# Kernel tuning notes

Measured on AMD Instinct MI355X. Metric: run time of the kernel, lower is better.

## Reference

```python
import jax, jax.numpy as jnp
import numpy as np

B, N, D, H, K, T = 32, 4096, 256, 4, 8, 3
D_H = D // H
SCALE = D_H ** -0.5
EPS = 1e-8
LN_EPS = 1e-5


def _ln(x, g, b):
    m = x.mean(-1, keepdims=True)
    v = ((x - m) ** 2).mean(-1, keepdims=True)
    return (x - m) / jnp.sqrt(v + LN_EPS) * g + b


def _split(t):  # [b, n, D] -> [b, H, n, d_h]
    b, n, _ = t.shape
    return t.reshape(b, n, H, D_H).transpose(0, 2, 1, 3)


def _merge(t):  # [b, H, n, d_h] -> [b, n, D]
    b, h, n, d = t.shape
    return t.transpose(0, 2, 1, 3).reshape(b, n, h * d)


def setup_inputs() -> dict:
    key = jax.random.key(0)
    ks = jax.random.split(key, 12)
    init = lambda k, shape: (jax.random.normal(k, shape, jnp.float32) * 0.02)
    mu = jnp.tile(jnp.linspace(-1.0, 1.0, K)[:, None], (1, D))[None]  # [1,K,D]
    return {
        'x': jax.random.normal(ks[0], (B, N, D), jnp.float32),
        'mu': mu,
        'w_q': init(ks[1], (D, D)),
        'w_k': init(ks[2], (D, D)),
        'w_v': init(ks[3], (D, D)),
        'w_comb': init(ks[4], (D, D)),
        'g_in': jnp.ones(D), 'b_in': jnp.zeros(D),
        'g_slot': jnp.ones(D), 'b_slot': jnp.zeros(D),
        'g_mlp': jnp.ones(D), 'b_mlp': jnp.zeros(D),
        'w_ih': init(ks[5], (3 * D, D)),
        'w_hh': init(ks[6], (3 * D, D)),
        'b_ih': jnp.zeros(3 * D),
        'b_hh': jnp.zeros(3 * D),
        'w1': init(ks[7], (D, D)), 'b1': jnp.zeros(D),
        'w2': init(ks[8], (D, D)), 'b2': jnp.zeros(D),
    }


def reference(x, mu, w_q, w_k, w_v, w_comb, g_in, b_in, g_slot, b_slot,
              g_mlp, b_mlp, w_ih, w_hh, b_ih, b_hh, w1, b1, w2, b2):
    b = x.shape[0]
    x_norm = _ln(x, g_in, b_in)
    k_feat = _split(x_norm @ w_k.T)  # [b,H,N,d_h]
    v_feat = _split(x_norm @ w_v.T)

    def gru(u, h):  # torch GRUCell semantics
        gi = u @ w_ih.T + b_ih
        gh = h @ w_hh.T + b_hh
        ir, iz, i_n = jnp.split(gi, 3, axis=-1)
        hr, hz, h_n = jnp.split(gh, 3, axis=-1)
        r = jax.nn.sigmoid(ir + hr)
        z = jax.nn.sigmoid(iz + hz)
        n = jnp.tanh(i_n + r * h_n)
        return (1.0 - z) * n + z * h

    def step(slots, _):
        q = _split(_ln(slots, g_slot, b_slot) @ w_q.T)  # [b,H,K,d_h]
        dots = jnp.einsum('bhkd,bhnd->bhkn', q, k_feat) * SCALE
        attn = jax.nn.softmax(dots, axis=-2)  # softmax over slots
        attn = attn / (attn.sum(axis=-1, keepdims=True) + EPS)  # renorm over inputs
        updates = _merge(jnp.einsum('bhkn,bhnd->bhkd', attn, v_feat)) @ w_comb.T
        new = gru(updates.reshape(-1, D), slots.reshape(-1, D)).reshape(slots.shape)
        hid = jnp.maximum(_ln(new, g_mlp, b_mlp) @ w1.T + b1, 0.0)
        new = new + (hid @ w2.T + b2)
        return new, None

    slots0 = jnp.broadcast_to(mu, (b, K, D))  # eval mode: slots = mu
    slots, _ = jax.lax.scan(step, slots0, None, length=T)
    return slots
```

## Files before the change

kernel.cpp:

```cpp
#include <hip/hip_runtime.h>

#define BB 32
#define NN 4096
#define DD 256
#define HH 4
#define KK 8
#define DH 64

typedef unsigned short u16;
typedef unsigned int u32;
typedef __attribute__((ext_vector_type(8))) short short8;
typedef __attribute__((ext_vector_type(4))) float f32x4;

__device__ __forceinline__ float b2f(u16 u){ return __uint_as_float(((u32)u)<<16); }
__device__ __forceinline__ u16 f2b(float f){
  u32 u = __float_as_uint(f);
  u32 r = (u + 0x7fffu + ((u>>16)&1u)) >> 16;
  return (u16)r;
}

__global__ __launch_bounds__(256) void prep_kernel(
    const float* __restrict__ mu, const float* __restrict__ w_q,
    const float* __restrict__ w_k, const float* __restrict__ w_v,
    const float* __restrict__ w_comb, const float* __restrict__ w_ih,
    const float* __restrict__ w_hh, const float* __restrict__ w1,
    const float* __restrict__ w2,
    u16* __restrict__ wkv, u16* __restrict__ wq_b, u16* __restrict__ wcomb_b,
    u16* __restrict__ wih_b, u16* __restrict__ whh_b, u16* __restrict__ w1_b,
    u16* __restrict__ w2_b, float* __restrict__ slots)
{
  int i = blockIdx.x*256 + threadIdx.x;
  if (i < 131072) {
    int c = i>>8, d = i&255;
    float v = (c<256) ? w_k[c*256+d] : w_v[(c-256)*256+d];
    int off = (c<<9) + ((2*d) ^ ((c&15)<<4));
    wkv[off>>1] = f2b(v);
    return;
  }
  i -= 131072;
  if (i < 65536){ wq_b[i] = f2b(w_q[i]); return; } i -= 65536;
  if (i < 65536){ wcomb_b[i] = f2b(w_comb[i]); return; } i -= 65536;
  if (i < 196608){ wih_b[i] = f2b(w_ih[i]); return; } i -= 196608;
  if (i < 196608){ whh_b[i] = f2b(w_hh[i]); return; } i -= 196608;
  if (i < 65536){ w1_b[i] = f2b(w1[i]); return; } i -= 65536;
  if (i < 65536){ w2_b[i] = f2b(w2[i]); return; } i -= 65536;
  if (i < 65536){ slots[i] = mu[i & 2047]; return; }
}

__global__ __launch_bounds__(512) void kv_proj_kernel(
    const float* __restrict__ x, const float* __restrict__ g_in,
    const float* __restrict__ b_in, const u16* __restrict__ wkv,
    u16* __restrict__ Kmat, u16* __restrict__ Vmat)
{
  __shared__ __align__(16) u16 Atile[64*256];
  __shared__ __align__(16) u16 Btile[64*256];
  __shared__ __align__(16) u16 Cbuf[64*64];
  const int tid = threadIdx.x;
  const int w = tid>>6, l = tid&63;
  const long row0 = (long)blockIdx.x * 64;

  short8 breg[4];
  #pragma unroll
  for (int i=0;i<4;++i)
    breg[i] = *(const short8*)((const char*)wkv + (i*512 + tid)*16);

  const f32x4 gv = *(const f32x4*)(g_in + l*4);
  const f32x4 bv = *(const f32x4*)(b_in + l*4);

  #pragma unroll
  for (int rr=0; rr<8; ++rr) {
    const int r = w*8 + rr;
    const f32x4 xv = *(const f32x4*)(x + (row0+r)*DD + l*4);
    float s = xv.x+xv.y+xv.z+xv.w;
    float s2 = xv.x*xv.x+xv.y*xv.y+xv.z*xv.z+xv.w*xv.w;
    #pragma unroll
    for (int m=1;m<64;m<<=1){ s += __shfl_xor(s,m); s2 += __shfl_xor(s2,m); }
    const float mean = s * (1.f/256.f);
    const float rstd = rsqrtf(s2*(1.f/256.f) - mean*mean + 1e-5f);
    const u32 p0 = (u32)f2b((xv.x-mean)*rstd*gv.x + bv.x) | ((u32)f2b((xv.y-mean)*rstd*gv.y + bv.y)<<16);
    const u32 p1 = (u32)f2b((xv.z-mean)*rstd*gv.z + bv.z) | ((u32)f2b((xv.w-mean)*rstd*gv.w + bv.w)<<16);
    const unsigned long long pp = (unsigned long long)p0 | ((unsigned long long)p1<<32);
    *(unsigned long long*)((char*)Atile + r*512 + ((l*8) ^ ((r&15)<<4))) = pp;
  }
  #pragma unroll
  for (int i=0;i<4;++i)
    *(short8*)((char*)Btile + (i*512+tid)*16) = breg[i];
  __syncthreads();

  const int wm = w>>2, wn = w&3;
  const int lr = l&15;
  const int lk = (l>>4)*8;

  for (int ct=0; ct<8; ++ct) {
    short8 nreg[4];
    if (ct < 7) {
      #pragma unroll
      for (int i=0;i<4;++i)
        nreg[i] = *(const short8*)((const char*)wkv + (ct+1)*32768 + (i*512 + tid)*16);
    }

    f32x4 acc0 = (f32x4)0.f, acc1 = (f32x4)0.f;
    #pragma unroll
    for (int ks=0; ks<8; ++ks) {
      const int k2 = (ks*32 + lk)*2;
      short8 af0, af1, bfv;
      { const int r = wm*32 + lr;       af0 = *(const short8*)((const char*)Atile + r*512 + (k2 ^ ((r&15)<<4))); }
      { const int r = wm*32 + 16 + lr;  af1 = *(const short8*)((const char*)Atile + r*512 + (k2 ^ ((r&15)<<4))); }
      { const int c = wn*16 + lr;       bfv = *(const short8*)((const char*)Btile + c*512 + (k2 ^ ((c&15)<<4))); }
      acc0 = __builtin_amdgcn_mfma_f32_16x16x32_bf16(af0, bfv, acc0, 0,0,0);
      acc1 = __builtin_amdgcn_mfma_f32_16x16x32_bf16(af1, bfv, acc1, 0,0,0);
    }

    {
      const int c = wn*16 + lr;
      #pragma unroll
      for (int reg=0; reg<4; ++reg) {
        const int r0r = wm*32 + (l>>4)*4 + reg;
        const int r1r = r0r + 16;
        *(u16*)((char*)Cbuf + r0r*128 + ((2*c) ^ ((r0r&7)<<4))) = f2b(acc0[reg]);
        *(u16*)((char*)Cbuf + r1r*128 + ((2*c) ^ ((r1r&7)<<4))) = f2b(acc1[reg]);
      }
    }
    __syncthreads();

    if (ct < 7) {
      #pragma unroll
      for (int i=0;i<4;++i)
        *(short8*)((char*)Btile + (i*512+tid)*16) = nreg[i];
    }
    {
      const int r = tid>>3, cg = tid&7;
      const short8 vv = *(const short8*)((char*)Cbuf + r*128 + ((cg*16) ^ ((r&7)<<4)));
      u16* dst = (ct<4) ? Kmat : Vmat;
      *(short8*)(dst + (row0+r)*DD + (ct&3)*64 + cg*8) = vv;
    }
    __syncthreads();
  }
}

__global__ __launch_bounds__(256) void slot_q_kernel(
    const float* __restrict__ slots, const float* __restrict__ g_slot,
    const float* __restrict__ b_slot, const u16* __restrict__ wq_b,
    float* __restrict__ qmat)
{
  __shared__ float xn[256];
  __shared__ float red[8];
  const int r = blockIdx.x, t = threadIdx.x;
  const int w = t>>6, l = t&63;
  const float xv = slots[r*256 + t];
  float s = xv, s2 = xv*xv;
  #pragma unroll
  for (int m=1;m<64;m<<=1){ s += __shfl_xor(s,m); s2 += __shfl_xor(s2,m); }
  if (l==0){ red[w*2]=s; red[w*2+1]=s2; }
  __syncthreads();
  s = red[0]+red[2]+red[4]+red[6];
  s2 = red[1]+red[3]+red[5]+red[7];
  const float mean = s*(1.f/256.f);
  const float rstd = rsqrtf(s2*(1.f/256.f)-mean*mean + 1e-5f);
  xn[t] = (xv-mean)*rstd*g_slot[t] + b_slot[t];
  __syncthreads();
  const u16* wr = wq_b + t*256;
  float a0=0,a1=0,a2=0,a3=0;
  for (int d=0; d<256; d+=8) {
    const short8 wv = *(const short8*)(wr + d);
    a0 = fmaf(b2f((u16)wv[0]), xn[d+0], a0);
    a1 = fmaf(b2f((u16)wv[1]), xn[d+1], a1);
    a2 = fmaf(b2f((u16)wv[2]), xn[d+2], a2);
    a3 = fmaf(b2f((u16)wv[3]), xn[d+3], a3);
    a0 = fmaf(b2f((u16)wv[4]), xn[d+4], a0);
    a1 = fmaf(b2f((u16)wv[5]), xn[d+5], a1);
    a2 = fmaf(b2f((u16)wv[6]), xn[d+6], a2);
    a3 = fmaf(b2f((u16)wv[7]), xn[d+7], a3);
  }
  qmat[r*256 + t] = ((a0+a1)+(a2+a3));
}

__global__ __launch_bounds__(256) void attn_kernel(
    const u16* __restrict__ Kmat, const u16* __restrict__ Vmat,
    const float* __restrict__ qmat, float* __restrict__ U_part,
    float* __restrict__ S_part)
{
  __shared__ float U_lds[4][8][64];
  __shared__ float S_lds[4][8];
  const int bid = blockIdx.x;
  const int part = bid & 3, h = (bid>>2)&3, b = bid>>4;
  const int t = threadIdx.x, w = t>>6, l = t&63;
  const int ds = l&7, ng = l>>3;

  float qreg[8][8];
  #pragma unroll
  for (int k=0;k<8;++k) {
    const f32x4 qa = *(const f32x4*)(qmat + (b*8+k)*256 + h*64 + ds*8);
    const f32x4 qb = *(const f32x4*)(qmat + (b*8+k)*256 + h*64 + ds*8 + 4);
    qreg[k][0]=qa.x; qreg[k][1]=qa.y; qreg[k][2]=qa.z; qreg[k][3]=qa.w;
    qreg[k][4]=qb.x; qreg[k][5]=qb.y; qreg[k][6]=qb.z; qreg[k][7]=qb.w;
  }

  float accU[8][8];
  float sacc[8];
  #pragma unroll
  for (int k=0;k<8;++k){ sacc[k]=0.f;
    #pragma unroll
    for (int j=0;j<8;++j) accU[k][j]=0.f; }

  const long base = ((long)b*NN)*DD + h*64;
  for (int pass=0; pass<32; ++pass) {
    const int n = part*1024 + pass*32 + w*8 + ng;
    const short8 kvv = *(const short8*)(Kmat + base + (long)n*DD + ds*8);
    float kd[8];
    #pragma unroll
    for (int j=0;j<8;++j) kd[j] = b2f((u16)kvv[j]);
    float dots[8];
    #pragma unroll
    for (int k=0;k<8;++k) {
      float d0 = qreg[k][0]*kd[0] + qreg[k][1]*kd[1] + qreg[k][2]*kd[2] + qreg[k][3]*kd[3]
               + qreg[k][4]*kd[4] + qreg[k][5]*kd[5] + qreg[k][6]*kd[6] + qreg[k][7]*kd[7];
      d0 += __shfl_xor(d0,1); d0 += __shfl_xor(d0,2); d0 += __shfl_xor(d0,4);
      dots[k] = d0 * 0.125f;
    }
    float mx = dots[0];
    #pragma unroll
    for (int k=1;k<8;++k) mx = fmaxf(mx, dots[k]);
    float e[8]; float se = 0.f;
    #pragma unroll
    for (int k=0;k<8;++k){ e[k] = __expf(dots[k]-mx); se += e[k]; }
    const float inv = 1.f/se;
    const short8 vvv = *(const short8*)(Vmat + base + (long)n*DD + ds*8);
    float vd[8];
    #pragma unroll
    for (int j=0;j<8;++j) vd[j] = b2f((u16)vvv[j]);
    #pragma unroll
    for (int k=0;k<8;++k) {
      const float p = e[k]*inv;
      sacc[k] += p;
      #pragma unroll
      for (int j=0;j<8;++j) accU[k][j] = fmaf(p, vd[j], accU[k][j]);
    }
  }
  #pragma unroll
  for (int k=0;k<8;++k){
    #pragma unroll
    for (int j=0;j<8;++j){
      float v = accU[k][j];
      v += __shfl_xor(v,8); v += __shfl_xor(v,16); v += __shfl_xor(v,32);
      accU[k][j]=v;
    }
    float sv = sacc[k];
    sv += __shfl_xor(sv,8); sv += __shfl_xor(sv,16); sv += __shfl_xor(sv,32);
    sacc[k]=sv;
  }
  if (l<8){
    #pragma unroll
    for (int k=0;k<8;++k)
      #pragma unroll
      for (int j=0;j<8;++j) U_lds[w][k][l*8+j] = accU[k][j];
  }
  if (l==0){
    #pragma unroll
    for (int k=0;k<8;++k) S_lds[w][k]=sacc[k];
  }
  __syncthreads();
  for (int i=t;i<512;i+=256){
    const int k=i>>6, d=i&63;
    U_part[(((long)part*32 + b)*4 + h)*512 + k*64 + d] =
      U_lds[0][k][d]+U_lds[1][k][d]+U_lds[2][k][d]+U_lds[3][k][d];
  }
  if (t<8){
    S_part[((part*32 + b)*4 + h)*8 + t] = S_lds[0][t]+S_lds[1][t]+S_lds[2][t]+S_lds[3][t];
  }
}

__global__ __launch_bounds__(256) void slot_update_kernel(
    const float* __restrict__ U_part, const float* __restrict__ S_part,
    float* __restrict__ slots,
    const u16* __restrict__ wcomb_b, const u16* __restrict__ wih_b,
    const u16* __restrict__ whh_b, const u16* __restrict__ w1_b,
    const u16* __restrict__ w2_b,
    const float* __restrict__ b_ih, const float* __restrict__ b_hh,
    const float* __restrict__ g_mlp, const float* __restrict__ b_mlp,
    const float* __restrict__ b1v, const float* __restrict__ b2v,
    float* __restrict__ out_final, const int write_out)
{
  __shared__ float uL[2][256];
  __shared__ float hL[2][256];
  __shared__ float cL[2][256];
  __shared__ float xL[2][256];
  __shared__ float red[16];
  const int blk = blockIdx.x, t = threadIdx.x;
  const int w = t>>6, l = t&63;
  const int r0 = blk*2;

  #pragma unroll
  for (int rr=0;rr<2;++rr) hL[rr][t] = slots[(r0+rr)*256 + t];

  #pragma unroll
  for (int rr=0;rr<2;++rr) {
    const int r = r0+rr, b = r>>3, k = r&7;
    const int h = t>>6, d = t&63;
    float ssum = 0.f, usum = 0.f;
    #pragma unroll
    for (int p=0;p<4;++p) {
      ssum += S_part[((p*32 + b)*4 + h)*8 + k];
      usum += U_part[(((long)p*32 + b)*4 + h)*512 + k*64 + d];
    }
    uL[rr][t] = usum / (ssum + 1e-8f);
  }
  __syncthreads();

  {
    float c00=0,c01=0,c10=0,c11=0;
    const u16* wr = wcomb_b + t*256;
    for (int d0=0; d0<256; d0+=8) {
      const short8 wv = *(const short8*)(wr + d0);
      float wf[8];
      #pragma unroll
      for (int j=0;j<8;++j) wf[j]=b2f((u16)wv[j]);
      #pragma unroll
      for (int j=0;j<8;j+=2) {
        c00 = fmaf(wf[j],   uL[0][d0+j],   c00);
        c01 = fmaf(wf[j+1], uL[0][d0+j+1], c01);
        c10 = fmaf(wf[j],   uL[1][d0+j],   c10);
        c11 = fmaf(wf[j+1], uL[1][d0+j+1], c11);
      }
    }
    cL[0][t]=c00+c01; cL[1][t]=c10+c11;
  }
  __syncthreads();

  float gi[3][2], gh[3][2];
  #pragma unroll
  for (int g=0; g<3; ++g){ gi[g][0]=0; gi[g][1]=0; gh[g][0]=0; gh[g][1]=0; }
  for (int d0=0; d0<256; d0+=8) {
    float u0[8],u1[8],h0[8],h1[8];
    #pragma unroll
    for (int j=0;j<8;j+=4) {
      *(f32x4*)&u0[j] = *(const f32x4*)&cL[0][d0+j];
      *(f32x4*)&u1[j] = *(const f32x4*)&cL[1][d0+j];
      *(f32x4*)&h0[j] = *(const f32x4*)&hL[0][d0+j];
      *(f32x4*)&h1[j] = *(const f32x4*)&hL[1][d0+j];
    }
    #pragma unroll
    for (int g=0; g<3; ++g) {
      const short8 wi = *(const short8*)(wih_b + (g*256+t)*256 + d0);
      const short8 wh = *(const short8*)(whh_b + (g*256+t)*256 + d0);
      #pragma unroll
      for (int j=0;j<8;++j) {
        const float a = b2f((u16)wi[j]);
        const float bw = b2f((u16)wh[j]);
        gi[g][0] = fmaf(a, u0[j], gi[g][0]);
        gi[g][1] = fmaf(a, u1[j], gi[g][1]);
        gh[g][0] = fmaf(bw, h0[j], gh[g][0]);
        gh[g][1] = fmaf(bw, h1[j], gh[g][1]);
      }
    }
  }
  float newv[2];
  #pragma unroll
  for (int rr=0;rr<2;++rr) {
    const float ir = gi[0][rr] + b_ih[t];
    const float iz = gi[1][rr] + b_ih[256+t];
    const float inn= gi[2][rr] + b_ih[512+t];
    const float hr = gh[0][rr] + b_hh[t];
    const float hz = gh[1][rr] + b_hh[256+t];
    const float hn = gh[2][rr] + b_hh[512+t];
    const float rg = 1.f/(1.f + __expf(-(ir+hr)));
    const float zg = 1.f/(1.f + __expf(-(iz+hz)));
    float targ = inn + rg*hn;
    targ = fminf(fmaxf(targ, -15.f), 15.f);
    const float ex = __expf(2.f*targ);
    const float ng = (ex-1.f)/(ex+1.f);
    newv[rr] = (1.f-zg)*ng + zg*hL[rr][t];
  }

  float s0=newv[0], q0=newv[0]*newv[0], s1=newv[1], q1=newv[1]*newv[1];
  #pragma unroll
  for (int m=1;m<64;m<<=1){
    s0+=__shfl_xor(s0,m); q0+=__shfl_xor(q0,m);
    s1+=__shfl_xor(s1,m); q1+=__shfl_xor(q1,m);
  }
  if (l==0){ red[w*4]=s0; red[w*4+1]=q0; red[w*4+2]=s1; red[w*4+3]=q1; }
  __syncthreads();
  s0 = red[0]+red[4]+red[8]+red[12];
  q0 = red[1]+red[5]+red[9]+red[13];
  s1 = red[2]+red[6]+red[10]+red[14];
  q1 = red[3]+red[7]+red[11]+red[15];
  {
    const float m0 = s0*(1.f/256.f), m1 = s1*(1.f/256.f);
    const float r0v = rsqrtf(q0*(1.f/256.f)-m0*m0 + 1e-5f);
    const float r1v = rsqrtf(q1*(1.f/256.f)-m1*m1 + 1e-5f);
    xL[0][t] = (newv[0]-m0)*r0v*g_mlp[t] + b_mlp[t];
    xL[1][t] = (newv[1]-m1)*r1v*g_mlp[t] + b_mlp[t];
  }
  __syncthreads();

  {
    float c00=0,c01=0,c10=0,c11=0;
    const u16* wr = w1_b + t*256;
    for (int d0=0; d0<256; d0+=8) {
      const short8 wv = *(const short8*)(wr + d0);
      float wf[8];
      #pragma unroll
      for (int j=0;j<8;++j) wf[j]=b2f((u16)wv[j]);
      #pragma unroll
      for (int j=0;j<8;j+=2) {
        c00 = fmaf(wf[j],   xL[0][d0+j],   c00);
        c01 = fmaf(wf[j+1], xL[0][d0+j+1], c01);
        c10 = fmaf(wf[j],   xL[1][d0+j],   c10);
        c11 = fmaf(wf[j+1], xL[1][d0+j+1], c11);
      }
    }
    uL[0][t] = fmaxf(c00+c01 + b1v[t], 0.f);
    uL[1][t] = fmaxf(c10+c11 + b1v[t], 0.f);
  }
  __syncthreads();

  {
    float c00=0,c01=0,c10=0,c11=0;
    const u16* wr = w2_b + t*256;
    for (int d0=0; d0<256; d0+=8) {
      const short8 wv = *(const short8*)(wr + d0);
      float wf[8];
      #pragma unroll
      for (int j=0;j<8;++j) wf[j]=b2f((u16)wv[j]);
      #pragma unroll
      for (int j=0;j<8;j+=2) {
        c00 = fmaf(wf[j],   uL[0][d0+j],   c00);
        c01 = fmaf(wf[j+1], uL[0][d0+j+1], c01);
        c10 = fmaf(wf[j],   uL[1][d0+j],   c10);
        c11 = fmaf(wf[j+1], uL[1][d0+j+1], c11);
      }
    }
    const float o0 = newv[0] + c00+c01 + b2v[t];
    const float o1 = newv[1] + c10+c11 + b2v[t];
    slots[(r0+0)*256 + t] = o0;
    slots[(r0+1)*256 + t] = o1;
    if (write_out){
      out_final[(r0+0)*256 + t] = o0;
      out_final[(r0+1)*256 + t] = o1;
    }
  }
}

extern "C" void kernel_launch(void* const* d_in, const int* in_sizes, int n_in,
                              void* d_out, int out_size, void* d_ws, size_t ws_size,
                              hipStream_t stream)
{
  (void)in_sizes; (void)n_in; (void)out_size; (void)ws_size;
  const float* x      = (const float*)d_in[0];
  const float* mu     = (const float*)d_in[1];
  const float* w_q    = (const float*)d_in[2];
  const float* w_k    = (const float*)d_in[3];
  const float* w_v    = (const float*)d_in[4];
  const float* w_comb = (const float*)d_in[5];
  const float* g_in   = (const float*)d_in[6];
  const float* b_in   = (const float*)d_in[7];
  const float* g_slot = (const float*)d_in[8];
  const float* b_slot = (const float*)d_in[9];
  const float* g_mlp  = (const float*)d_in[10];
  const float* b_mlp  = (const float*)d_in[11];
  const float* w_ih   = (const float*)d_in[12];
  const float* w_hh   = (const float*)d_in[13];
  const float* b_ih   = (const float*)d_in[14];
  const float* b_hh   = (const float*)d_in[15];
  const float* w1     = (const float*)d_in[16];
  const float* b1     = (const float*)d_in[17];
  const float* w2     = (const float*)d_in[18];
  const float* b2     = (const float*)d_in[19];

  char* ws = (char*)d_ws;
  u16* Kmat    = (u16*)(ws + 0);
  u16* Vmat    = (u16*)(ws + 67108864);
  u16* wkv     = (u16*)(ws + 134217728);
  u16* wq_b    = (u16*)(ws + 134479872);
  u16* wcomb_b = (u16*)(ws + 134610944);
  u16* wih_b   = (u16*)(ws + 134742016);
  u16* whh_b   = (u16*)(ws + 135135232);
  u16* w1_b    = (u16*)(ws + 135528448);
  u16* w2_b    = (u16*)(ws + 135659520);
  float* slots = (float*)(ws + 135790592);
  float* qmat  = (float*)(ws + 136052736);
  float* U_part= (float*)(ws + 136314880);
  float* S_part= (float*)(ws + 137363456);

  hipLaunchKernelGGL(prep_kernel, dim3(3328), dim3(256), 0, stream,
                     mu, w_q, w_k, w_v, w_comb, w_ih, w_hh, w1, w2,
                     wkv, wq_b, wcomb_b, wih_b, whh_b, w1_b, w2_b, slots);
  hipLaunchKernelGGL(kv_proj_kernel, dim3(2048), dim3(512), 0, stream,
                     x, g_in, b_in, wkv, Kmat, Vmat);
  float* outp = (float*)d_out;
  for (int it=0; it<3; ++it) {
    hipLaunchKernelGGL(slot_q_kernel, dim3(256), dim3(256), 0, stream,
                       slots, g_slot, b_slot, wq_b, qmat);
    hipLaunchKernelGGL(attn_kernel, dim3(512), dim3(256), 0, stream,
                       Kmat, Vmat, qmat, U_part, S_part);
    hipLaunchKernelGGL(slot_update_kernel, dim3(128), dim3(256), 0, stream,
                       U_part, S_part, slots, wcomb_b, wih_b, whh_b, w1_b, w2_b,
                       b_ih, b_hh, g_mlp, b_mlp, b1, b2, outp, (it==2)?1:0);
  }
}
```

Baseline: 368.1 us.

## Keep KV-proj operands in registers, prefetch attention loads, fuse slot Q projection

The K/V projection kernel drops its shared-memory B tile. It loads weight fragments straight from global memory into registers, preloads the A fragments once, and double-buffers the output staging buffer, which removes one barrier per column tile. The attention kernel software-prefetches the next K/V row into registers. The slot query projection for iterations two and three is fused into the tail of the slot update kernel, which saves two launches. The costs are higher register pressure and uncoalesced direct global loads of the weights.

```diff
diff --git a/kernel.cpp b/kernel.cpp
--- a/kernel.cpp
+++ b/kernel.cpp
@@ -31,10 +31,7 @@
 {
   int i = blockIdx.x*256 + threadIdx.x;
   if (i < 131072) {
-    int c = i>>8, d = i&255;
-    float v = (c<256) ? w_k[c*256+d] : w_v[(c-256)*256+d];
-    int off = (c<<9) + ((2*d) ^ ((c&15)<<4));
-    wkv[off>>1] = f2b(v);
+    wkv[i] = f2b((i < 65536) ? w_k[i] : w_v[i-65536]);
     return;
   }
   i -= 131072;
@@ -47,22 +44,28 @@
   if (i < 65536){ slots[i] = mu[i & 2047]; return; }
 }
 
-__global__ __launch_bounds__(512) void kv_proj_kernel(
+__global__ __launch_bounds__(512,4) void kv_proj_kernel(
     const float* __restrict__ x, const float* __restrict__ g_in,
     const float* __restrict__ b_in, const u16* __restrict__ wkv,
     u16* __restrict__ Kmat, u16* __restrict__ Vmat)
 {
   __shared__ __align__(16) u16 Atile[64*256];
-  __shared__ __align__(16) u16 Btile[64*256];
-  __shared__ __align__(16) u16 Cbuf[64*64];
+  __shared__ __align__(16) u16 Cbuf[2][64*64];
   const int tid = threadIdx.x;
   const int w = tid>>6, l = tid&63;
   const long row0 = (long)blockIdx.x * 64;
-
-  short8 breg[4];
-  #pragma unroll
-  for (int i=0;i<4;++i)
-    breg[i] = *(const short8*)((const char*)wkv + (i*512 + tid)*16);
+  const int wm = w>>2, wn = w&3;
+  const int lr = l&15, lk = (l>>4)*8;
+
+  const u16* bp = wkv + (wn*16 + lr)*256 + lk;
+  short8 bf[8];
+  #pragma unroll
+  for (int ks=0;ks<8;++ks) bf[ks] = *(const short8*)(bp + ks*32);
+
+  f32x4 xr[8];
+  #pragma unroll
+  for (int rr=0;rr<8;++rr)
+    xr[rr] = *(const f32x4*)(x + (row0 + w*8 + rr)*DD + l*4);
 
   const f32x4 gv = *(const f32x4*)(g_in + l*4);
   const f32x4 bv = *(const f32x4*)(b_in + l*4);
@@ -70,7 +73,7 @@
   #pragma unroll
   for (int rr=0; rr<8; ++rr) {
     const int r = w*8 + rr;
-    const f32x4 xv = *(const f32x4*)(x + (row0+r)*DD + l*4);
+    const f32x4 xv = xr[rr];
     float s = xv.x+xv.y+xv.z+xv.w;
     float s2 = xv.x*xv.x+xv.y*xv.y+xv.z*xv.z+xv.w*xv.w;
     #pragma unroll
@@ -82,33 +85,35 @@
     const unsigned long long pp = (unsigned long long)p0 | ((unsigned long long)p1<<32);
     *(unsigned long long*)((char*)Atile + r*512 + ((l*8) ^ ((r&15)<<4))) = pp;
   }
-  #pragma unroll
-  for (int i=0;i<4;++i)
-    *(short8*)((char*)Btile + (i*512+tid)*16) = breg[i];
-  __syncthreads();
-
-  const int wm = w>>2, wn = w&3;
-  const int lr = l&15;
-  const int lk = (l>>4)*8;
-
+  __syncthreads();
+
+  short8 afr0[8], afr1[8];
+  #pragma unroll
+  for (int ks=0;ks<8;++ks) {
+    const int k2 = (ks*32 + lk)*2;
+    { const int r = wm*32 + lr;      afr0[ks] = *(const short8*)((const char*)Atile + r*512 + (k2 ^ ((r&15)<<4))); }
+    { const int r = wm*32 + 16 + lr; afr1[ks] = *(const short8*)((const char*)Atile + r*512 + (k2 ^ ((r&15)<<4))); }
+  }
+
+  #pragma unroll
   for (int ct=0; ct<8; ++ct) {
-    short8 nreg[4];
+    if (ct > 0) {
+      const int r = tid>>3, cg = tid&7;
+      const short8 vv = *(const short8*)((char*)Cbuf[(ct-1)&1] + r*128 + ((cg*16) ^ ((r&7)<<4)));
+      u16* dst = ((ct-1)<4) ? Kmat : Vmat;
+      *(short8*)(dst + (row0+r)*DD + ((ct-1)&3)*64 + cg*8) = vv;
+    }
+
+    f32x4 acc0 = (f32x4)0.f, acc1 = (f32x4)0.f;
+    #pragma unroll
+    for (int ks=0;ks<8;++ks) {
+      acc0 = __builtin_amdgcn_mfma_f32_16x16x32_bf16(afr0[ks], bf[ks], acc0, 0,0,0);
+      acc1 = __builtin_amdgcn_mfma_f32_16x16x32_bf16(afr1[ks], bf[ks], acc1, 0,0,0);
+    }
+
     if (ct < 7) {
       #pragma unroll
-      for (int i=0;i<4;++i)
-        nreg[i] = *(const short8*)((const char*)wkv + (ct+1)*32768 + (i*512 + tid)*16);
-    }
-
-    f32x4 acc0 = (f32x4)0.f, acc1 = (f32x4)0.f;
-    #pragma unroll
-    for (int ks=0; ks<8; ++ks) {
-      const int k2 = (ks*32 + lk)*2;
-      short8 af0, af1, bfv;
-      { const int r = wm*32 + lr;       af0 = *(const short8*)((const char*)Atile + r*512 + (k2 ^ ((r&15)<<4))); }
-      { const int r = wm*32 + 16 + lr;  af1 = *(const short8*)((const char*)Atile + r*512 + (k2 ^ ((r&15)<<4))); }
-      { const int c = wn*16 + lr;       bfv = *(const short8*)((const char*)Btile + c*512 + (k2 ^ ((c&15)<<4))); }
-      acc0 = __builtin_amdgcn_mfma_f32_16x16x32_bf16(af0, bfv, acc0, 0,0,0);
-      acc1 = __builtin_amdgcn_mfma_f32_16x16x32_bf16(af1, bfv, acc1, 0,0,0);
+      for (int ks=0;ks<8;++ks) bf[ks] = *(const short8*)(bp + (ct+1)*16384 + ks*32);
     }
 
     {
@@ -117,24 +122,16 @@
       for (int reg=0; reg<4; ++reg) {
         const int r0r = wm*32 + (l>>4)*4 + reg;
         const int r1r = r0r + 16;
-        *(u16*)((char*)Cbuf + r0r*128 + ((2*c) ^ ((r0r&7)<<4))) = f2b(acc0[reg]);
-        *(u16*)((char*)Cbuf + r1r*128 + ((2*c) ^ ((r1r&7)<<4))) = f2b(acc1[reg]);
+        *(u16*)((char*)Cbuf[ct&1] + r0r*128 + ((2*c) ^ ((r0r&7)<<4))) = f2b(acc0[reg]);
+        *(u16*)((char*)Cbuf[ct&1] + r1r*128 + ((2*c) ^ ((r1r&7)<<4))) = f2b(acc1[reg]);
       }
     }
     __syncthreads();
-
-    if (ct < 7) {
-      #pragma unroll
-      for (int i=0;i<4;++i)
-        *(short8*)((char*)Btile + (i*512+tid)*16) = nreg[i];
-    }
-    {
-      const int r = tid>>3, cg = tid&7;
-      const short8 vv = *(const short8*)((char*)Cbuf + r*128 + ((cg*16) ^ ((r&7)<<4)));
-      u16* dst = (ct<4) ? Kmat : Vmat;
-      *(short8*)(dst + (row0+r)*DD + (ct&3)*64 + cg*8) = vv;
-    }
-    __syncthreads();
+  }
+  {
+    const int r = tid>>3, cg = tid&7;
+    const short8 vv = *(const short8*)((char*)Cbuf[1] + r*128 + ((cg*16) ^ ((r&7)<<4)));
+    *(short8*)(Vmat + (row0+r)*DD + 3*64 + cg*8) = vv;
   }
 }
 
@@ -204,12 +201,20 @@
     for (int j=0;j<8;++j) accU[k][j]=0.f; }
 
   const long base = ((long)b*NN)*DD + h*64;
+  const u16* Kp = Kmat + base + (long)(part*1024 + w*8 + ng)*DD + ds*8;
+  const u16* Vp = Vmat + base + (long)(part*1024 + w*8 + ng)*DD + ds*8;
+
+  short8 kc = *(const short8*)Kp;
+  short8 vc = *(const short8*)Vp;
   for (int pass=0; pass<32; ++pass) {
-    const int n = part*1024 + pass*32 + w*8 + ng;
-    const short8 kvv = *(const short8*)(Kmat + base + (long)n*DD + ds*8);
+    short8 kn, vn;
+    if (pass < 31) {
+      kn = *(const short8*)(Kp + (pass+1)*32*DD);
+      vn = *(const short8*)(Vp + (pass+1)*32*DD);
+    }
     float kd[8];
     #pragma unroll
-    for (int j=0;j<8;++j) kd[j] = b2f((u16)kvv[j]);
+    for (int j=0;j<8;++j) kd[j] = b2f((u16)kc[j]);
     float dots[8];
     #pragma unroll
     for (int k=0;k<8;++k) {
@@ -225,10 +230,9 @@
     #pragma unroll
     for (int k=0;k<8;++k){ e[k] = __expf(dots[k]-mx); se += e[k]; }
     const float inv = 1.f/se;
-    const short8 vvv = *(const short8*)(Vmat + base + (long)n*DD + ds*8);
     float vd[8];
     #pragma unroll
-    for (int j=0;j<8;++j) vd[j] = b2f((u16)vvv[j]);
+    for (int j=0;j<8;++j) vd[j] = b2f((u16)vc[j]);
     #pragma unroll
     for (int k=0;k<8;++k) {
       const float p = e[k]*inv;
@@ -236,6 +240,7 @@
       #pragma unroll
       for (int j=0;j<8;++j) accU[k][j] = fmaf(p, vd[j], accU[k][j]);
     }
+    kc = kn; vc = vn;
   }
   #pragma unroll
   for (int k=0;k<8;++k){
@@ -279,7 +284,9 @@
     const float* __restrict__ b_ih, const float* __restrict__ b_hh,
     const float* __restrict__ g_mlp, const float* __restrict__ b_mlp,
     const float* __restrict__ b1v, const float* __restrict__ b2v,
-    float* __restrict__ out_final, const int write_out)
+    const u16* __restrict__ wq_b, const float* __restrict__ g_slot,
+    const float* __restrict__ b_slot, float* __restrict__ qmat,
+    float* __restrict__ out_final, const int write_out, const int compute_q)
 {
   __shared__ float uL[2][256];
   __shared__ float hL[2][256];
@@ -414,6 +421,7 @@
   }
   __syncthreads();
 
+  float o0, o1;
   {
     float c00=0,c01=0,c10=0,c11=0;
     const u16* wr = w2_b + t*256;
@@ -430,14 +438,53 @@
         c11 = fmaf(wf[j+1], uL[1][d0+j+1], c11);
       }
     }
-    const float o0 = newv[0] + c00+c01 + b2v[t];
-    const float o1 = newv[1] + c10+c11 + b2v[t];
+    o0 = newv[0] + c00+c01 + b2v[t];
+    o1 = newv[1] + c10+c11 + b2v[t];
     slots[(r0+0)*256 + t] = o0;
     slots[(r0+1)*256 + t] = o1;
     if (write_out){
       out_final[(r0+0)*256 + t] = o0;
       out_final[(r0+1)*256 + t] = o1;
     }
+  }
+
+  if (compute_q) {
+    __syncthreads();
+    float t0=o0, p0=o0*o0, t1=o1, p1=o1*o1;
+    #pragma unroll
+    for (int m=1;m<64;m<<=1){
+      t0+=__shfl_xor(t0,m); p0+=__shfl_xor(p0,m);
+      t1+=__shfl_xor(t1,m); p1+=__shfl_xor(p1,m);
+    }
+    if (l==0){ red[w*4]=t0; red[w*4+1]=p0; red[w*4+2]=t1; red[w*4+3]=p1; }
+    __syncthreads();
+    t0 = red[0]+red[4]+red[8]+red[12];
+    p0 = red[1]+red[5]+red[9]+red[13];
+    t1 = red[2]+red[6]+red[10]+red[14];
+    p1 = red[3]+red[7]+red[11]+red[15];
+    const float m0 = t0*(1.f/256.f), m1 = t1*(1.f/256.f);
+    const float r0v = rsqrtf(p0*(1.f/256.f)-m0*m0 + 1e-5f);
+    const float r1v = rsqrtf(p1*(1.f/256.f)-m1*m1 + 1e-5f);
+    cL[0][t] = (o0-m0)*r0v*g_slot[t] + b_slot[t];
+    cL[1][t] = (o1-m1)*r1v*g_slot[t] + b_slot[t];
+    __syncthreads();
+    float c00=0,c01=0,c10=0,c11=0;
+    const u16* wr = wq_b + t*256;
+    for (int d0=0; d0<256; d0+=8) {
+      const short8 wv = *(const short8*)(wr + d0);
+      float wf[8];
+      #pragma unroll
+      for (int j=0;j<8;++j) wf[j]=b2f((u16)wv[j]);
+      #pragma unroll
+      for (int j=0;j<8;j+=2) {
+        c00 = fmaf(wf[j],   cL[0][d0+j],   c00);
+        c01 = fmaf(wf[j+1], cL[0][d0+j+1], c01);
+        c10 = fmaf(wf[j],   cL[1][d0+j],   c10);
+        c11 = fmaf(wf[j+1], cL[1][d0+j+1], c11);
+      }
+    }
+    qmat[(r0+0)*256 + t] = c00+c01;
+    qmat[(r0+1)*256 + t] = c10+c11;
   }
 }
 
@@ -487,14 +534,16 @@
                      wkv, wq_b, wcomb_b, wih_b, whh_b, w1_b, w2_b, slots);
   hipLaunchKernelGGL(kv_proj_kernel, dim3(2048), dim3(512), 0, stream,
                      x, g_in, b_in, wkv, Kmat, Vmat);
+  hipLaunchKernelGGL(slot_q_kernel, dim3(256), dim3(256), 0, stream,
+                     slots, g_slot, b_slot, wq_b, qmat);
   float* outp = (float*)d_out;
   for (int it=0; it<3; ++it) {
-    hipLaunchKernelGGL(slot_q_kernel, dim3(256), dim3(256), 0, stream,
-                       slots, g_slot, b_slot, wq_b, qmat);
     hipLaunchKernelGGL(attn_kernel, dim3(512), dim3(256), 0, stream,
                        Kmat, Vmat, qmat, U_part, S_part);
     hipLaunchKernelGGL(slot_update_kernel, dim3(128), dim3(256), 0, stream,
                        U_part, S_part, slots, wcomb_b, wih_b, whh_b, w1_b, w2_b,
-                       b_ih, b_hh, g_mlp, b_mlp, b1, b2, outp, (it==2)?1:0);
-  }
-}
+                       b_ih, b_hh, g_mlp, b_mlp, b1, b2,
+                       wq_b, g_slot, b_slot, qmat,
+                       outp, (it==2)?1:0, (it<2)?1:0);
+  }
+}
```

Result: slower. 412.3 us (+12.0%).
